# Performance work log

Measured on AMD Instinct MI355X. Metric: run time of the kernel, lower is better.

The kernel has to match this reference:

```python
import jax, jax.numpy as jnp
import numpy as np

N = 262144      # total tokens
LM1 = 6         # max digit chars after the first character
D = 128         # embedding_dim
NUM_LAB = 1000
V1 = 2 * 26 + NUM_LAB  # first-level table rows (1052)


def setup_inputs() -> dict:
    key = jax.random.key(0)
    k1, k2, k3, k4, k5, k6, k7 = jax.random.split(key, 7)
    return {
        "first_chars": jax.random.randint(k1, (N,), 0, 26, dtype=jnp.int32),
        "digits": jax.random.randint(k2, (N, LM1), 0, 10, dtype=jnp.int32),
        "ndigits": jax.random.randint(k3, (N,), 0, 7, dtype=jnp.int32),
        "mods": jax.random.randint(k4, (N,), 0, 3, dtype=jnp.int32),  # 0=icd10,1=atc,2=lab
        "vals": jax.random.normal(k5, (N,), dtype=jnp.float32),
        "E1": jax.random.normal(k6, (V1, D), dtype=jnp.float32),
        "Eint": jax.random.normal(k7, (10, D), dtype=jnp.float32),
        "kappa": 2,
    }


def reference(first_chars, digits, ndigits, mods, vals, E1, Eint, kappa):
    # first-level index per modality: icd -> c+5, atc -> 2c+5, lab -> 52+code
    first_idx = jnp.where(
        mods == 0, first_chars + 5,
        jnp.where(mods == 1, first_chars * 2 + 5, 52 + first_chars))
    base = E1[first_idx]                                  # [N, D]

    # position-decayed digit accumulation: sum_i 1/(i+2)^kappa * Eint[digit_i]
    pos = jnp.arange(LM1, dtype=jnp.float32)
    w = 1.0 / (pos + 2.0) ** kappa                        # [LM1]
    mask = (jnp.arange(LM1)[None, :] < ndigits[:, None]).astype(base.dtype)
    onehot = jax.nn.one_hot(digits, 10, dtype=base.dtype)  # [N, LM1, 10]
    digit_emb = jnp.einsum("nl,nlk,kd->nd", w[None, :] * mask, onehot, Eint)

    # modality scatter: lab tokens use base * val, icd/atc use base + decayed digits
    final = jnp.where((mods == 2)[:, None], base * vals[:, None], base + digit_emb)
    return final
```

## Files before the change

kernel.cpp:

```cpp
#include <hip/hip_runtime.h>
#include <hip/hip_bf16.h>


#define LM1 6
#define D   128
#define TPB 128

typedef float nfloat4 __attribute__((ext_vector_type(4)));
typedef int   nint4   __attribute__((ext_vector_type(4)));

__global__ __launch_bounds__(256, 8) void hier_emb_kernel(
    const int*   __restrict__ first_chars,
    const int*   __restrict__ digits,
    const int*   __restrict__ ndigits,
    const int*   __restrict__ mods,
    const float* __restrict__ vals,
    const float* __restrict__ E1,
    const float* __restrict__ Eint,
    const int*   __restrict__ kappa_p,
    float*       __restrict__ out,
    int n)
{
    __shared__ float sEint[10][D];
    __shared__ nint4 sMeta[TPB];
    __shared__ int   sDig[TPB * LM1];

    const int tid  = threadIdx.x;
    const int tok0 = blockIdx.x * TPB;

    {
        const nfloat4* src = reinterpret_cast<const nfloat4*>(Eint);
        nfloat4*       dst = reinterpret_cast<nfloat4*>(&sEint[0][0]);
        dst[tid] = src[tid];
        const int i2 = 256 + tid;
        if (i2 < (10 * D) / 4) dst[i2] = src[i2];
    }
    {
        const long lim = (long)n * LM1;
#pragma unroll
        for (int r = 0; r < (TPB * LM1) / 256; ++r) {
            const int i = tid + r * 256;
            long gi = (long)tok0 * LM1 + i;
            if (gi >= lim) gi = lim - 1;
            sDig[i] = digits[gi];
        }
    }
    if (tid < TPB) {
        int tt = tok0 + tid; if (tt >= n) tt = n - 1;
        const int mod  = mods[tt];
        const int fc   = first_chars[tt];
        const int fidx = (mod == 0) ? fc + 5 : (mod == 1) ? fc * 2 + 5 : 52 + fc;
        const int nd   = (mod == 2) ? 0 : ndigits[tt];
        const float v  = (mod == 2) ? vals[tt] : 1.0f;
        nint4 m; m.x = fidx; m.y = 0; m.z = nd; m.w = __float_as_int(v);
        sMeta[tid] = m;
    }

    const int k = *kappa_p;
    float w[LM1];
#pragma unroll
    for (int i = 0; i < LM1; ++i) {
        float p = 1.0f;
        const float b = (float)(i + 2);
        for (int j = 0; j < k; ++j) p *= b;
        w[i] = 1.0f / p;
    }

    __syncthreads();

    if (tid < TPB) {
        int pd = 0;
#pragma unroll
        for (int i = 0; i < LM1; ++i) pd |= sDig[tid * LM1 + i] << (4 * i);
        reinterpret_cast<int*>(sMeta)[tid * 4 + 1] = pd;
    }
    __syncthreads();

    const int q4 = (tid & 31) * 4;
    const int h  = (tid >> 5) & 1;
    const int wv = tid >> 6;
    const int tb = wv * 32;

    const float* E1Q   = E1 + q4;
    const float* EintQ = &sEint[0][q4];
    float*       outQ  = out + q4;


    nint4 m0 = sMeta[tb + h];
    nint4 m1 = sMeta[tb + h + 2];
    nfloat4 b0 = *reinterpret_cast<const nfloat4*>(E1Q + (size_t)m0.x * D);
    nfloat4 b1 = *reinterpret_cast<const nfloat4*>(E1Q + (size_t)m1.x * D);

#pragma unroll
    for (int g = 0; g < 8; ++g) {
        nint4 p0, p1; nfloat4 c0, c1;
        if (g < 7) {
            const int ln = tb + (g + 1) * 4 + h;
            p0 = sMeta[ln];
            p1 = sMeta[ln + 2];
            c0 = *reinterpret_cast<const nfloat4*>(E1Q + (size_t)p0.x * D);
            c1 = *reinterpret_cast<const nfloat4*>(E1Q + (size_t)p1.x * D);
        }

        const int ltA = tb + g * 4 + h;
        {
            nfloat4 acc = b0 * __int_as_float(m0.w);
            const int nd = m0.z, pd = m0.y;
#pragma unroll
            for (int i = 0; i < LM1; ++i) {
                if (i < nd) {
                    const int dg = (pd >> (4 * i)) & 15;
                    acc += w[i] * *reinterpret_cast<const nfloat4*>(EintQ + dg * D);
                }
            }
            const int tok = tok0 + ltA;
            if (tok < n)
                __builtin_nontemporal_store(
                    acc, reinterpret_cast<nfloat4*>(outQ + (size_t)tok * D));
        }
        {
            nfloat4 acc = b1 * __int_as_float(m1.w);
            const int nd = m1.z, pd = m1.y;
#pragma unroll
            for (int i = 0; i < LM1; ++i) {
                if (i < nd) {
                    const int dg = (pd >> (4 * i)) & 15;
                    acc += w[i] * *reinterpret_cast<const nfloat4*>(EintQ + dg * D);
                }
            }
            const int tok = tok0 + ltA + 2;
            if (tok < n)
                __builtin_nontemporal_store(
                    acc, reinterpret_cast<nfloat4*>(outQ + (size_t)tok * D));
        }
        m0 = p0; m1 = p1; b0 = c0; b1 = c1;
    }
}

extern "C" void kernel_launch(void* const* d_in, const int* in_sizes, int n_in,
                              void* d_out, int out_size, void* d_ws, size_t ws_size,
                              hipStream_t stream) {
    const int*   first_chars = (const int*)  d_in[0];
    const int*   digits      = (const int*)  d_in[1];
    const int*   ndigits     = (const int*)  d_in[2];
    const int*   mods        = (const int*)  d_in[3];
    const float* vals        = (const float*)d_in[4];
    const float* E1          = (const float*)d_in[5];
    const float* Eint        = (const float*)d_in[6];
    const int*   kappa       = (const int*)  d_in[7];
    float*       out         = (float*)d_out;

    const int n    = in_sizes[0];
    const int grid = (n + TPB - 1) / TPB;

    hier_emb_kernel<<<grid, 256, 0, stream>>>(
        first_chars, digits, ndigits, mods, vals, E1, Eint, kappa, out, n);
}
```

Measured before the change: 161.5 us.

## Pack digits directly per token, deepen E1 prefetch, specialize unguarded full blocks

Each metadata thread now reads its token's six digits as three int2 loads and packs them itself. This removes the shared digit staging buffer and one block barrier. The output loop is restructured into 16 single-token steps with a 4-deep register ring of prefetched E1 rows and metadata, instead of 8 steps with one-step lookahead. Full blocks take a template-specialized path without bounds checks. In exchange there are more live registers, launch bounds drop to 6 waves per SIMD, and the int2 digit loads are strided across threads and less coalesced.

```diff
diff --git a/kernel.cpp b/kernel.cpp
--- a/kernel.cpp
+++ b/kernel.cpp
@@ -2,14 +2,19 @@
 #include <hip/hip_bf16.h>
 
 
-#define LM1 6
-#define D   128
-#define TPB 128
+#define LM1   6
+#define D     128
+#define TPB   128
+#define NGRP  16
+#define DEPTH 4
 
 typedef float nfloat4 __attribute__((ext_vector_type(4)));
 typedef int   nint4   __attribute__((ext_vector_type(4)));
+typedef int   nint2   __attribute__((ext_vector_type(2)));
 
-__global__ __launch_bounds__(256, 8) void hier_emb_kernel(
+template <bool B> struct BoolC { static constexpr bool value = B; };
+
+__global__ __launch_bounds__(256, 6) void hier_emb_kernel(
     const int*   __restrict__ first_chars,
     const int*   __restrict__ digits,
     const int*   __restrict__ ndigits,
@@ -23,7 +28,6 @@
 {
     __shared__ float sEint[10][D];
     __shared__ nint4 sMeta[TPB];
-    __shared__ int   sDig[TPB * LM1];
 
     const int tid  = threadIdx.x;
     const int tok0 = blockIdx.x * TPB;
@@ -35,16 +39,6 @@
         const int i2 = 256 + tid;
         if (i2 < (10 * D) / 4) dst[i2] = src[i2];
     }
-    {
-        const long lim = (long)n * LM1;
-#pragma unroll
-        for (int r = 0; r < (TPB * LM1) / 256; ++r) {
-            const int i = tid + r * 256;
-            long gi = (long)tok0 * LM1 + i;
-            if (gi >= lim) gi = lim - 1;
-            sDig[i] = digits[gi];
-        }
-    }
     if (tid < TPB) {
         int tt = tok0 + tid; if (tt >= n) tt = n - 1;
         const int mod  = mods[tt];
@@ -52,7 +46,11 @@
         const int fidx = (mod == 0) ? fc + 5 : (mod == 1) ? fc * 2 + 5 : 52 + fc;
         const int nd   = (mod == 2) ? 0 : ndigits[tt];
         const float v  = (mod == 2) ? vals[tt] : 1.0f;
-        nint4 m; m.x = fidx; m.y = 0; m.z = nd; m.w = __float_as_int(v);
+        const nint2* dp = reinterpret_cast<const nint2*>(digits + (size_t)tt * LM1);
+        const nint2 d01 = dp[0], d23 = dp[1], d45 = dp[2];
+        const int pd = d01.x | (d01.y << 4) | (d23.x << 8) | (d23.y << 12)
+                     | (d45.x << 16) | (d45.y << 20);
+        nint4 m; m.x = fidx; m.y = pd; m.z = nd; m.w = __float_as_int(v);
         sMeta[tid] = m;
     }
 
@@ -68,44 +66,35 @@
 
     __syncthreads();
 
-    if (tid < TPB) {
-        int pd = 0;
-#pragma unroll
-        for (int i = 0; i < LM1; ++i) pd |= sDig[tid * LM1 + i] << (4 * i);
-        reinterpret_cast<int*>(sMeta)[tid * 4 + 1] = pd;
-    }
-    __syncthreads();
-
     const int q4 = (tid & 31) * 4;
     const int h  = (tid >> 5) & 1;
-    const int wv = tid >> 6;
-    const int tb = wv * 32;
+    const int tb = (tid >> 6) * 32;
 
     const float* E1Q   = E1 + q4;
     const float* EintQ = &sEint[0][q4];
     float*       outQ  = out + q4;
 
-
-    nint4 m0 = sMeta[tb + h];
-    nint4 m1 = sMeta[tb + h + 2];
-    nfloat4 b0 = *reinterpret_cast<const nfloat4*>(E1Q + (size_t)m0.x * D);
-    nfloat4 b1 = *reinterpret_cast<const nfloat4*>(E1Q + (size_t)m1.x * D);
-
+    auto hot = [&](auto guard_c) {
+        constexpr bool GUARD = decltype(guard_c)::value;
+        nint4   m[DEPTH];
+        nfloat4 b[DEPTH];
 #pragma unroll
-    for (int g = 0; g < 8; ++g) {
-        nint4 p0, p1; nfloat4 c0, c1;
-        if (g < 7) {
-            const int ln = tb + (g + 1) * 4 + h;
-            p0 = sMeta[ln];
-            p1 = sMeta[ln + 2];
-            c0 = *reinterpret_cast<const nfloat4*>(E1Q + (size_t)p0.x * D);
-            c1 = *reinterpret_cast<const nfloat4*>(E1Q + (size_t)p1.x * D);
+        for (int p = 0; p < DEPTH; ++p) {
+            m[p] = sMeta[tb + p * 2 + h];
+            b[p] = *reinterpret_cast<const nfloat4*>(E1Q + (size_t)m[p].x * D);
         }
-
-        const int ltA = tb + g * 4 + h;
-        {
-            nfloat4 acc = b0 * __int_as_float(m0.w);
-            const int nd = m0.z, pd = m0.y;
+#pragma unroll
+        for (int g = 0; g < NGRP; ++g) {
+            const int s = g & (DEPTH - 1);
+            const nint4   mm = m[s];
+            const nfloat4 bb = b[s];
+            if (g + DEPTH < NGRP) {
+                m[s] = sMeta[tb + (g + DEPTH) * 2 + h];
+                b[s] = *reinterpret_cast<const nfloat4*>(
+                           E1Q + (size_t)m[s].x * D);
+            }
+            nfloat4 acc = bb * __int_as_float(mm.w);
+            const int nd = mm.z, pd = mm.y;
 #pragma unroll
             for (int i = 0; i < LM1; ++i) {
                 if (i < nd) {
@@ -113,28 +102,16 @@
                     acc += w[i] * *reinterpret_cast<const nfloat4*>(EintQ + dg * D);
                 }
             }
-            const int tok = tok0 + ltA;
-            if (tok < n)
+            const int tok = tok0 + tb + g * 2 + h;
+            if (!GUARD || tok < n) {
                 __builtin_nontemporal_store(
                     acc, reinterpret_cast<nfloat4*>(outQ + (size_t)tok * D));
+            }
         }
-        {
-            nfloat4 acc = b1 * __int_as_float(m1.w);
-            const int nd = m1.z, pd = m1.y;
-#pragma unroll
-            for (int i = 0; i < LM1; ++i) {
-                if (i < nd) {
-                    const int dg = (pd >> (4 * i)) & 15;
-                    acc += w[i] * *reinterpret_cast<const nfloat4*>(EintQ + dg * D);
-                }
-            }
-            const int tok = tok0 + ltA + 2;
-            if (tok < n)
-                __builtin_nontemporal_store(
-                    acc, reinterpret_cast<nfloat4*>(outQ + (size_t)tok * D));
-        }
-        m0 = p0; m1 = p1; b0 = c0; b1 = c1;
-    }
+    };
+
+    if (tok0 + TPB <= n) hot(BoolC<false>{});
+    else                 hot(BoolC<true>{});
 }
 
 extern "C" void kernel_launch(void* const* d_in, const int* in_sizes, int n_in,
```

Result: slower. 202.4 us (+25.3%).
